# Kernel tuning notes

Measured on AMD Instinct MI355X. Metric: run time of the kernel, lower is better.

Reference implementation:

```python
import jax, jax.numpy as jnp
import numpy as np

DT = 0.01
NJ = 7
GRAV = 9.81
Q_LOWER = jnp.array([-2.9671, -1.8326, -2.9671, -3.1416, -2.9671, -0.0873, -2.9671], jnp.float32)
Q_UPPER = jnp.array([ 2.9671,  1.8326,  2.9671,  0.0,     2.9671,  3.8223,  2.9671], jnp.float32)


def _skew(v):
    z = jnp.zeros((), v.dtype)
    return jnp.stack([jnp.stack([z, -v[2], v[1]]),
                      jnp.stack([v[2], z, -v[0]]),
                      jnp.stack([-v[1], v[0], z])])


def _mot_X(E, r):
    # 6x6 spatial motion transform [[E,0],[-E*skew(r),E]]
    zero = jnp.zeros_like(E)
    top = jnp.concatenate([E, zero], axis=1)
    bot = jnp.concatenate([-E @ _skew(r), E], axis=1)
    return jnp.concatenate([top, bot], axis=0)


def _crm(v):
    # spatial motion cross-product matrix for v=[w;v0]
    Sw, Sv = _skew(v[:3]), _skew(v[3:])
    zero = jnp.zeros_like(Sw)
    top = jnp.concatenate([Sw, zero], axis=1)
    bot = jnp.concatenate([Sv, Sw], axis=1)
    return jnp.concatenate([top, bot], axis=0)


def _step_single(x, u, axes, R_tree, p_tree, I_sp):
    dt_ = x.dtype
    q = jnp.clip(x[:NJ], Q_LOWER.astype(dt_), Q_UPPER.astype(dt_))
    qd = x[NJ:]
    # forward kinematics: per-joint 6x6 child<-parent transforms and motion subspaces
    Xups, Ss = [], []
    eye3 = jnp.eye(3, dtype=dt_)
    for i in range(NJ):
        a = axes[i]
        c, s = jnp.cos(q[i]), jnp.sin(q[i])
        R = c * eye3 + s * _skew(a) + (1.0 - c) * jnp.outer(a, a)  # rodrigues
        Xj = _mot_X(R.T, jnp.zeros(3, dt_))
        Xt = _mot_X(R_tree[i], p_tree[i])
        Xups.append(Xj @ Xt)
        Ss.append(jnp.concatenate([a, jnp.zeros(3, dt_)]))
    # RNEA bias force h (qdd=0, gravity, zero base velocity, identity base pose)
    v_prev = jnp.zeros(6, dt_)
    a_prev = jnp.array([0.0, 0.0, 0.0, 0.0, 0.0, GRAV], dt_)  # a_base = -g trick
    fs = []
    for i in range(NJ):
        vJ = Ss[i] * qd[i]
        v = Xups[i] @ v_prev + vJ
        acc = Xups[i] @ a_prev + _crm(v) @ vJ
        Iv = I_sp[i] @ v
        f = I_sp[i] @ acc - _crm(v).T @ Iv  # crf(v) = -crm(v)^T
        fs.append(f)
        v_prev, a_prev = v, acc
    h = [None] * NJ
    for i in range(NJ - 1, -1, -1):
        h[i] = Ss[i] @ fs[i]
        if i > 0:
            fs[i - 1] = fs[i - 1] + Xups[i].T @ fs[i]
    h = jnp.stack(h)
    # CRBA mass matrix (serial chain, parent(i)=i-1)
    Ic = [I_sp[i] for i in range(NJ)]
    M = jnp.zeros((NJ, NJ), dt_)
    for i in range(NJ - 1, -1, -1):
        if i > 0:
            Ic[i - 1] = Ic[i - 1] + Xups[i].T @ Ic[i] @ Xups[i]
        F = Ic[i] @ Ss[i]
        M = M.at[i, i].set(Ss[i] @ F)
        for j in range(i - 1, -1, -1):
            F = Xups[j + 1].T @ F
            mij = Ss[j] @ F
            M = M.at[i, j].set(mij).at[j, i].set(mij)
    M = M + 1e-8 * jnp.eye(NJ, dtype=dt_)
    qdd = jnp.linalg.solve(M, (u - h)[:, None])[:, 0]
    qd_new = qd + DT * qdd
    q_new = q + DT * qd_new
    return jnp.concatenate([q_new, qd_new])


def setup_inputs() -> dict:
    B = 65536
    key = jax.random.key(0)
    k1, k2 = jax.random.split(key)
    x = jax.random.normal(k1, (B, 14), jnp.float32)
    u = jax.random.normal(k2, (B, 7), jnp.float32)
    rng = np.random.default_rng(0)
    # unit joint axes
    axes = rng.normal(size=(NJ, 3))
    axes = axes / np.linalg.norm(axes, axis=1, keepdims=True)
    # orthonormal fixed parent->child rotations (det +1)
    R_tree = np.empty((NJ, 3, 3))
    for i in range(NJ):
        Q, _ = np.linalg.qr(rng.normal(size=(3, 3)))
        if np.linalg.det(Q) < 0:
            Q[:, 0] = -Q[:, 0]
        R_tree[i] = Q
    p_tree = 0.2 * rng.normal(size=(NJ, 3))
    # SPD 6x6 spatial inertias: [[Ibar, m*Cx],[m*Cx^T, m*I3]]
    I_sp = np.empty((NJ, 6, 6))
    for i in range(NJ):
        m = float(rng.uniform(1.0, 5.0))
        c = 0.05 * rng.normal(size=3)
        Cx = np.array([[0, -c[2], c[1]], [c[2], 0, -c[0]], [-c[1], c[0], 0]])
        A = 0.1 * rng.normal(size=(3, 3))
        Ic_ = A @ A.T + 0.05 * np.eye(3)
        Ibar = Ic_ + m * Cx @ Cx.T
        I_sp[i] = np.block([[Ibar, m * Cx], [m * Cx.T, m * np.eye(3)]])
    return {
        "x": x, "u": u,
        "axes": jnp.asarray(axes, jnp.float32),
        "R_tree": jnp.asarray(R_tree, jnp.float32),
        "p_tree": jnp.asarray(p_tree, jnp.float32),
        "I_sp": jnp.asarray(I_sp, jnp.float32),
    }


def reference(x, u, axes, R_tree, p_tree, I_sp):
    return jax.vmap(_step_single, in_axes=(0, 0, None, None, None, None))(
        x, u, axes, R_tree, p_tree, I_sp)
```

## Files before the change

### kernel.cpp

```cpp
#include <hip/hip_runtime.h>
#include <math.h>

#define NJ 7
#define DTF 0.01f
#define GRAVF 9.81f
#define MIX(i,j) ((i)*((i)+1)/2 + (j))
#define MPAD 29
#define FSTR 43
#define SNC  15
#define QST  9

__device__ __forceinline__ void cross3(const float* a, const float* b, float* o){
    o[0] = a[1]*b[2] - a[2]*b[1];
    o[1] = a[2]*b[0] - a[0]*b[2];
    o[2] = a[0]*b[1] - a[1]*b[0];
}
__device__ __forceinline__ void mv3(const float* E, const float* x, float* y){
    y[0] = E[0]*x[0] + E[1]*x[1] + E[2]*x[2];
    y[1] = E[3]*x[0] + E[4]*x[1] + E[5]*x[2];
    y[2] = E[6]*x[0] + E[7]*x[1] + E[8]*x[2];
}
__device__ __forceinline__ void mtv3(const float* E, const float* x, float* y){
    y[0] = E[0]*x[0] + E[3]*x[1] + E[6]*x[2];
    y[1] = E[1]*x[0] + E[4]*x[1] + E[7]*x[2];
    y[2] = E[2]*x[0] + E[5]*x[1] + E[8]*x[2];
}
__device__ __forceinline__ void symv(const float* S, const float* x, float* y){
    y[0] = S[0]*x[0] + S[1]*x[1] + S[2]*x[2];
    y[1] = S[1]*x[0] + S[3]*x[1] + S[4]*x[2];
    y[2] = S[2]*x[0] + S[4]*x[1] + S[5]*x[2];
}
__device__ __forceinline__ void mm3(const float* A, const float* B, float* o){
#pragma unroll
    for (int r = 0; r < 3; r++)
#pragma unroll
        for (int c = 0; c < 3; c++)
            o[r*3+c] = A[r*3]*B[c] + A[r*3+1]*B[3+c] + A[r*3+2]*B[6+c];
}
__device__ __forceinline__ void congr(const float* E, const float* X, float* o){
    float t[9];
#pragma unroll
    for (int r = 0; r < 3; r++)
#pragma unroll
        for (int c = 0; c < 3; c++)
            t[r*3+c] = E[r]*X[c] + E[3+r]*X[3+c] + E[6+r]*X[6+c];
    mm3(t, E, o);
}
__device__ __forceinline__ void makeE(const float* a, const float* __restrict__ Rt,
                                      float s, float c, float* E){
    float omc = 1.0f - c;
    float RT[9];
    RT[0] = c + omc*a[0]*a[0];       RT[1] =  s*a[2] + omc*a[0]*a[1]; RT[2] = -s*a[1] + omc*a[0]*a[2];
    RT[3] = -s*a[2] + omc*a[1]*a[0]; RT[4] = c + omc*a[1]*a[1];       RT[5] =  s*a[0] + omc*a[1]*a[2];
    RT[6] =  s*a[1] + omc*a[2]*a[0]; RT[7] = -s*a[0] + omc*a[2]*a[1]; RT[8] = c + omc*a[2]*a[2];
    float Rl[9];
#pragma unroll
    for (int k = 0; k < 9; k++) Rl[k] = Rt[k];
    mm3(RT, Rl, E);
}
__device__ __forceinline__ void bodyI(const float* __restrict__ g_I, int i,
                                      float* SA, float* h, float& m){
    const float* I6 = g_I + i*36;
    SA[0]=I6[0]; SA[1]=I6[1]; SA[2]=I6[2];
    SA[3]=I6[7]; SA[4]=I6[8]; SA[5]=I6[14];
    h[0]=I6[16]; h[1]=I6[5]; h[2]=I6[9];
    m = I6[21];
}

__constant__ float QL_c[NJ] = {-2.9671f,-1.8326f,-2.9671f,-3.1416f,-2.9671f,-0.0873f,-2.9671f};
__constant__ float QU_c[NJ] = { 2.9671f, 1.8326f, 2.9671f, 0.0f,    2.9671f, 3.8223f, 2.9671f};

__global__ __launch_bounds__(128)
void panda_step(const float* __restrict__ x, const float* __restrict__ u,
                const float* __restrict__ g_ax, const float* __restrict__ g_Rt,
                const float* __restrict__ g_pt, const float* __restrict__ g_I,
                float* __restrict__ out, int B)
{
    __shared__ float s_M[64*MPAD];
    __shared__ float s_F[2*64*FSTR];
    __shared__ float s_snc[64*SNC];
    __shared__ float s_qd[64*QST];
    __shared__ float s_rhs[64*QST];

    const int role = threadIdx.x >> 6;
    const int lane = threadIdx.x & 63;
    const int e    = blockIdx.x*64 + lane;
    const bool act = (e < B);

    float q[NJ], qd[NJ];
    if (act && role == 0){
        float xl[14];
        const float2* x2 = (const float2*)(x + e*14);
#pragma unroll
        for (int i = 0; i < 7; i++){ float2 v = x2[i]; xl[2*i] = v.x; xl[2*i+1] = v.y; }
#pragma unroll
        for (int i = 0; i < NJ; i++){
            q[i]  = fminf(fmaxf(xl[i], QL_c[i]), QU_c[i]);
            qd[i] = xl[NJ + i];
            float s, c; __sincosf(q[i], &s, &c);
            s_snc[lane*SNC + i]     = s;
            s_snc[lane*SNC + 7 + i] = c;
            s_qd[lane*QST + i]      = qd[i];
            s_rhs[lane*QST + i]     = u[e*NJ + i];
        }
    }
    __syncthreads();

    if (act && role == 1){
        float* Fb = &s_F[64*FSTR + lane*FSTR];
        float SA[6], hc[3], mc;
        bodyI(g_I, 6, SA, hc, mc);
#pragma unroll 1
        for (int i = NJ-1; i >= 0; --i){
            float a[3] = { g_ax[3*i], g_ax[3*i+1], g_ax[3*i+2] };
            float p[3] = { g_pt[3*i], g_pt[3*i+1], g_pt[3*i+2] };
            float Ft[3]; symv(SA, a, Ft);
            Fb[i*6+0]=Ft[0]; Fb[i*6+1]=Ft[1]; Fb[i*6+2]=Ft[2];
            Fb[i*6+3] = a[1]*hc[2] - a[2]*hc[1];
            Fb[i*6+4] = a[2]*hc[0] - a[0]*hc[2];
            Fb[i*6+5] = a[0]*hc[1] - a[1]*hc[0];
#pragma unroll 1
            for (int k = i; k < NJ; ++k){
                float f0=Fb[k*6], f1=Fb[k*6+1], f2=Fb[k*6+2];
                s_M[lane*MPAD + k*(k+1)/2 + i] = a[0]*f0 + a[1]*f1 + a[2]*f2;
            }
            if (i > 0){
                float snv = s_snc[lane*SNC+i], csv = s_snc[lane*SNC+7+i];
                float E[9]; makeE(a, g_Rt + 9*i, snv, csv, E);
                float SAm[6], hm[3], mm_;
                bodyI(g_I, i-1, SAm, hm, mm_);
                float Af[9] = {SA[0],SA[1],SA[2], SA[1],SA[3],SA[4], SA[2],SA[4],SA[5]};
                float Ap[9]; congr(E, Af, Ap);
                float hr[3]; mtv3(E, hc, hr);
                float hpd = hr[0]*p[0]+hr[1]*p[1]+hr[2]*p[2];
                float ppd = p[0]*p[0]+p[1]*p[1]+p[2]*p[2];
                float dga = 2.0f*hpd + mc*ppd;
                SA[0] = Ap[0] - 2.0f*p[0]*hr[0] - mc*p[0]*p[0] + dga + SAm[0];
                SA[1] = Ap[1] - p[0]*hr[1] - hr[0]*p[1] - mc*p[0]*p[1] + SAm[1];
                SA[2] = Ap[2] - p[0]*hr[2] - hr[0]*p[2] - mc*p[0]*p[2] + SAm[2];
                SA[3] = Ap[4] - 2.0f*p[1]*hr[1] - mc*p[1]*p[1] + dga + SAm[3];
                SA[4] = Ap[5] - p[1]*hr[2] - hr[1]*p[2] - mc*p[1]*p[2] + SAm[4];
                SA[5] = Ap[8] - 2.0f*p[2]*hr[2] - mc*p[2]*p[2] + dga + SAm[5];
                hc[0] = hr[0] + mc*p[0] + hm[0];
                hc[1] = hr[1] + mc*p[1] + hm[1];
                hc[2] = hr[2] + mc*p[2] + hm[2];
                mc += mm_;
#pragma unroll 1
                for (int k = i; k < NJ; ++k){
                    float ft[3] = {Fb[k*6+0], Fb[k*6+1], Fb[k*6+2]};
                    float fb[3] = {Fb[k*6+3], Fb[k*6+4], Fb[k*6+5]};
                    float tm[3], tf[3], cp[3];
                    mtv3(E, ft, tm); mtv3(E, fb, tf);
                    cross3(p, tf, cp);
                    Fb[k*6+0]=tm[0]+cp[0]; Fb[k*6+1]=tm[1]+cp[1]; Fb[k*6+2]=tm[2]+cp[2];
                    Fb[k*6+3]=tf[0];       Fb[k*6+4]=tf[1];       Fb[k*6+5]=tf[2];
                }
            }
        }
        float Mx[28];
#pragma unroll
        for (int j = 0; j < 28; j++) Mx[j] = s_M[lane*MPAD + j];
#pragma unroll
        for (int i = 0; i < NJ; i++) Mx[MIX(i,i)] += 1e-8f;
#pragma unroll
        for (int k = 0; k < NJ; k++){
            float d = Mx[MIX(k,k)];
#pragma unroll
            for (int j = 0; j < NJ; j++) if (j < k) d -= Mx[MIX(k,j)]*Mx[MIX(k,j)];
            float linv = __builtin_amdgcn_rsqf(d);
            Mx[MIX(k,k)] = linv;
#pragma unroll
            for (int i2 = k+1; i2 < NJ; i2++){
                float s2 = Mx[MIX(i2,k)];
#pragma unroll
                for (int j = 0; j < NJ; j++) if (j < k) s2 -= Mx[MIX(i2,j)]*Mx[MIX(k,j)];
                Mx[MIX(i2,k)] = s2 * linv;
            }
        }
#pragma unroll
        for (int j = 0; j < 28; j++) s_M[lane*MPAD + j] = Mx[j];
    }
    else if (act){
        float* Fb = &s_F[lane*FSTR];
        float w[3]  = {0.f,0.f,0.f}, vl[3] = {0.f,0.f,0.f};
        float aw[3] = {0.f,0.f,0.f}, av[3] = {0.f,0.f,GRAVF};
#pragma unroll 1
        for (int i = 0; i < NJ; ++i){
            float a[3] = { g_ax[3*i], g_ax[3*i+1], g_ax[3*i+2] };
            float p[3] = { g_pt[3*i], g_pt[3*i+1], g_pt[3*i+2] };
            float snv = s_snc[lane*SNC+i], csv = s_snc[lane*SNC+7+i];
            float qdi = s_qd[lane*QST+i];
            float E[9]; makeE(a, g_Rt + 9*i, snv, csv, E);
            float tw[3]; mv3(E, w, tw);
            float nw[3] = { tw[0]+a[0]*qdi, tw[1]+a[1]*qdi, tw[2]+a[2]*qdi };
            float cwp[3]; cross3(w, p, cwp);
            float t1[3] = { vl[0]+cwp[0], vl[1]+cwp[1], vl[2]+cwp[2] };
            float nvl[3]; mv3(E, t1, nvl);
            float taw[3]; mv3(E, aw, taw);
            float cna[3]; cross3(nw, a, cna);
            float naw[3] = { taw[0]+qdi*cna[0], taw[1]+qdi*cna[1], taw[2]+qdi*cna[2] };
            float cap[3]; cross3(aw, p, cap);
            float t2[3] = { av[0]+cap[0], av[1]+cap[1], av[2]+cap[2] };
            float tav[3]; mv3(E, t2, tav);
            float cva[3]; cross3(nvl, a, cva);
            float nav[3] = { tav[0]+qdi*cva[0], tav[1]+qdi*cva[1], tav[2]+qdi*cva[2] };
            float SAi[6], hi[3], mi; bodyI(g_I, i, SAi, hi, mi);
            float Ivt[3], Iat[3], hxv[3], hxa[3];
            symv(SAi, nw, Ivt);  cross3(hi, nvl, hxv);
            symv(SAi, naw, Iat); cross3(hi, nav, hxa);
#pragma unroll
            for (int k = 0; k < 3; k++){ Ivt[k] += hxv[k]; Iat[k] += hxa[k]; }
            float hxw[3], hxaw[3];
            cross3(hi, nw, hxw); cross3(hi, naw, hxaw);
            float Ivb[3] = { mi*nvl[0]-hxw[0], mi*nvl[1]-hxw[1], mi*nvl[2]-hxw[2] };
            float Iab[3] = { mi*nav[0]-hxaw[0], mi*nav[1]-hxaw[1], mi*nav[2]-hxaw[2] };
            float c1[3], c2[3], c3[3];
            cross3(nw, Ivt, c1); cross3(nvl, Ivb, c2); cross3(nw, Ivb, c3);
            Fb[i*6+0] = Iat[0]+c1[0]+c2[0];
            Fb[i*6+1] = Iat[1]+c1[1]+c2[1];
            Fb[i*6+2] = Iat[2]+c1[2]+c2[2];
            Fb[i*6+3] = Iab[0]+c3[0];
            Fb[i*6+4] = Iab[1]+c3[1];
            Fb[i*6+5] = Iab[2]+c3[2];
#pragma unroll
            for (int k = 0; k < 3; k++){ w[k]=nw[k]; vl[k]=nvl[k]; aw[k]=naw[k]; av[k]=nav[k]; }
        }
#pragma unroll 1
        for (int i = NJ-1; i >= 0; --i){
            float a[3] = { g_ax[3*i], g_ax[3*i+1], g_ax[3*i+2] };
            float f0=Fb[i*6+0], f1=Fb[i*6+1], f2=Fb[i*6+2];
            s_rhs[lane*QST+i] -= a[0]*f0 + a[1]*f1 + a[2]*f2;
            if (i > 0){
                float p[3] = { g_pt[3*i], g_pt[3*i+1], g_pt[3*i+2] };
                float snv = s_snc[lane*SNC+i], csv = s_snc[lane*SNC+7+i];
                float E[9]; makeE(a, g_Rt + 9*i, snv, csv, E);
                float ftop[3] = {f0, f1, f2};
                float fbot[3] = {Fb[i*6+3], Fb[i*6+4], Fb[i*6+5]};
                float tm[3], tf[3], cp[3];
                mtv3(E, ftop, tm); mtv3(E, fbot, tf);
                cross3(p, tf, cp);
                Fb[(i-1)*6+0] += tm[0]+cp[0];
                Fb[(i-1)*6+1] += tm[1]+cp[1];
                Fb[(i-1)*6+2] += tm[2]+cp[2];
                Fb[(i-1)*6+3] += tf[0];
                Fb[(i-1)*6+4] += tf[1];
                Fb[(i-1)*6+5] += tf[2];
            }
        }
    }

    __syncthreads();

    if (act && role == 0){
        float Mx[28];
#pragma unroll
        for (int j = 0; j < 28; j++) Mx[j] = s_M[lane*MPAD + j];
        float rhs[NJ];
#pragma unroll
        for (int i = 0; i < NJ; i++) rhs[i] = s_rhs[lane*QST + i];
        float y[NJ];
#pragma unroll
        for (int i = 0; i < NJ; i++){
            float s2 = rhs[i];
#pragma unroll
            for (int j = 0; j < NJ; j++) if (j < i) s2 -= Mx[MIX(i,j)]*y[j];
            y[i] = s2 * Mx[MIX(i,i)];
        }
        float z[NJ];
#pragma unroll
        for (int i = NJ-1; i >= 0; i--){
            float s2 = y[i];
#pragma unroll
            for (int j = NJ-1; j >= 0; j--) if (j > i) s2 -= Mx[MIX(j,i)]*z[j];
            z[i] = s2 * Mx[MIX(i,i)];
        }
        float o14[14];
#pragma unroll
        for (int i = 0; i < NJ; i++){
            float qdn = qd[i] + DTF*z[i];
            o14[i]      = q[i] + DTF*qdn;
            o14[NJ + i] = qdn;
        }
        float2* o2 = (float2*)(out + e*14);
#pragma unroll
        for (int i = 0; i < 7; i++){ float2 v; v.x = o14[2*i]; v.y = o14[2*i+1]; o2[i] = v; }
    }
}

extern "C" void kernel_launch(void* const* d_in, const int* in_sizes, int n_in,
                              void* d_out, int out_size, void* d_ws, size_t ws_size,
                              hipStream_t stream) {
    const float* x   = (const float*)d_in[0];
    const float* u   = (const float*)d_in[1];
    const float* ax  = (const float*)d_in[2];
    const float* Rt  = (const float*)d_in[3];
    const float* pt  = (const float*)d_in[4];
    const float* Isp = (const float*)d_in[5];
    float* out = (float*)d_out;
    int B = in_sizes[0] / 14;
    int grid = (B + 63) / 64;
    hipLaunchKernelGGL(panda_step, dim3(grid), dim3(128), 0, stream,
                       x, u, ax, Rt, pt, Isp, out, B);
}
```

Measured before the change: 78.58 us.

## Replace RNEA+CRBA+Cholesky with Featherstone articulated-body algorithm per thread

```diff
diff --git a/kernel.cpp b/kernel.cpp
--- a/kernel.cpp
+++ b/kernel.cpp
@@ -4,11 +4,16 @@
 #define NJ 7
 #define DTF 0.01f
 #define GRAVF 9.81f
-#define MIX(i,j) ((i)*((i)+1)/2 + (j))
-#define MPAD 29
-#define FSTR 43
-#define SNC  15
-#define QST  9
+
+#define S_SN(i)    (i)
+#define S_CS(i)    (7 + (i))
+#define S_QD(i)    (14 + (i))
+#define S_TAU(i)   (21 + (i))
+#define S_VU(i,k)  (28 + 6*(i) + (k))
+#define S_CC(i,k)  (70 + 6*(i) + (k))
+#define S_DI(i)    (112 + (i))
+#define S_UU(i)    (119 + (i))
+#define NSLOT 126
 
 __device__ __forceinline__ void cross3(const float* a, const float* b, float* o){
     o[0] = a[1]*b[2] - a[2]*b[1];
@@ -37,14 +42,38 @@
         for (int c = 0; c < 3; c++)
             o[r*3+c] = A[r*3]*B[c] + A[r*3+1]*B[3+c] + A[r*3+2]*B[6+c];
 }
+__device__ __forceinline__ void mtm3(const float* A, const float* B, float* o){
+#pragma unroll
+    for (int r = 0; r < 3; r++)
+#pragma unroll
+        for (int c = 0; c < 3; c++)
+            o[r*3+c] = A[r]*B[c] + A[3+r]*B[3+c] + A[6+r]*B[6+c];
+}
 __device__ __forceinline__ void congr(const float* E, const float* X, float* o){
     float t[9];
-#pragma unroll
-    for (int r = 0; r < 3; r++)
-#pragma unroll
-        for (int c = 0; c < 3; c++)
-            t[r*3+c] = E[r]*X[c] + E[3+r]*X[3+c] + E[6+r]*X[6+c];
+    mtm3(E, X, t);
     mm3(t, E, o);
+}
+__device__ __forceinline__ void skewR(const float* M, const float* p, float* O){
+#pragma unroll
+    for (int r = 0; r < 3; r++){
+        O[r*3+0] = M[r*3+1]*p[2] - M[r*3+2]*p[1];
+        O[r*3+1] = M[r*3+2]*p[0] - M[r*3+0]*p[2];
+        O[r*3+2] = M[r*3+0]*p[1] - M[r*3+1]*p[0];
+    }
+}
+__device__ __forceinline__ void skewL(const float* p, const float* M, float* O){
+#pragma unroll
+    for (int c = 0; c < 3; c++){
+        O[0*3+c] = p[1]*M[2*3+c] - p[2]*M[1*3+c];
+        O[1*3+c] = p[2]*M[0*3+c] - p[0]*M[2*3+c];
+        O[2*3+c] = p[0]*M[1*3+c] - p[1]*M[0*3+c];
+    }
+}
+__device__ __forceinline__ void symexp(const float* S, float* F){
+    F[0]=S[0]; F[1]=S[1]; F[2]=S[2];
+    F[3]=S[1]; F[4]=S[3]; F[5]=S[4];
+    F[6]=S[2]; F[7]=S[4]; F[8]=S[5];
 }
 __device__ __forceinline__ void makeE(const float* a, const float* __restrict__ Rt,
                                       float s, float c, float* E){
@@ -70,25 +99,20 @@
 __constant__ float QL_c[NJ] = {-2.9671f,-1.8326f,-2.9671f,-3.1416f,-2.9671f,-0.0873f,-2.9671f};
 __constant__ float QU_c[NJ] = { 2.9671f, 1.8326f, 2.9671f, 0.0f,    2.9671f, 3.8223f, 2.9671f};
 
-__global__ __launch_bounds__(128)
+__global__ __launch_bounds__(64, 1)
 void panda_step(const float* __restrict__ x, const float* __restrict__ u,
                 const float* __restrict__ g_ax, const float* __restrict__ g_Rt,
                 const float* __restrict__ g_pt, const float* __restrict__ g_I,
                 float* __restrict__ out, int B)
 {
-    __shared__ float s_M[64*MPAD];
-    __shared__ float s_F[2*64*FSTR];
-    __shared__ float s_snc[64*SNC];
-    __shared__ float s_qd[64*QST];
-    __shared__ float s_rhs[64*QST];
-
-    const int role = threadIdx.x >> 6;
-    const int lane = threadIdx.x & 63;
+    __shared__ float s_buf[NSLOT*64];
+    const int lane = threadIdx.x;
     const int e    = blockIdx.x*64 + lane;
-    const bool act = (e < B);
+    if (e >= B) return;
+#define SL(idx) s_buf[(idx)*64 + lane]
 
     float q[NJ], qd[NJ];
-    if (act && role == 0){
+    {
         float xl[14];
         const float2* x2 = (const float2*)(x + e*14);
 #pragma unroll
@@ -98,186 +122,167 @@
             q[i]  = fminf(fmaxf(xl[i], QL_c[i]), QU_c[i]);
             qd[i] = xl[NJ + i];
             float s, c; __sincosf(q[i], &s, &c);
-            s_snc[lane*SNC + i]     = s;
-            s_snc[lane*SNC + 7 + i] = c;
-            s_qd[lane*QST + i]      = qd[i];
-            s_rhs[lane*QST + i]     = u[e*NJ + i];
-        }
-    }
-    __syncthreads();
-
-    if (act && role == 1){
-        float* Fb = &s_F[64*FSTR + lane*FSTR];
-        float SA[6], hc[3], mc;
-        bodyI(g_I, 6, SA, hc, mc);
-#pragma unroll 1
-        for (int i = NJ-1; i >= 0; --i){
-            float a[3] = { g_ax[3*i], g_ax[3*i+1], g_ax[3*i+2] };
-            float p[3] = { g_pt[3*i], g_pt[3*i+1], g_pt[3*i+2] };
-            float Ft[3]; symv(SA, a, Ft);
-            Fb[i*6+0]=Ft[0]; Fb[i*6+1]=Ft[1]; Fb[i*6+2]=Ft[2];
-            Fb[i*6+3] = a[1]*hc[2] - a[2]*hc[1];
-            Fb[i*6+4] = a[2]*hc[0] - a[0]*hc[2];
-            Fb[i*6+5] = a[0]*hc[1] - a[1]*hc[0];
-#pragma unroll 1
-            for (int k = i; k < NJ; ++k){
-                float f0=Fb[k*6], f1=Fb[k*6+1], f2=Fb[k*6+2];
-                s_M[lane*MPAD + k*(k+1)/2 + i] = a[0]*f0 + a[1]*f1 + a[2]*f2;
-            }
-            if (i > 0){
-                float snv = s_snc[lane*SNC+i], csv = s_snc[lane*SNC+7+i];
-                float E[9]; makeE(a, g_Rt + 9*i, snv, csv, E);
-                float SAm[6], hm[3], mm_;
-                bodyI(g_I, i-1, SAm, hm, mm_);
-                float Af[9] = {SA[0],SA[1],SA[2], SA[1],SA[3],SA[4], SA[2],SA[4],SA[5]};
-                float Ap[9]; congr(E, Af, Ap);
-                float hr[3]; mtv3(E, hc, hr);
-                float hpd = hr[0]*p[0]+hr[1]*p[1]+hr[2]*p[2];
-                float ppd = p[0]*p[0]+p[1]*p[1]+p[2]*p[2];
-                float dga = 2.0f*hpd + mc*ppd;
-                SA[0] = Ap[0] - 2.0f*p[0]*hr[0] - mc*p[0]*p[0] + dga + SAm[0];
-                SA[1] = Ap[1] - p[0]*hr[1] - hr[0]*p[1] - mc*p[0]*p[1] + SAm[1];
-                SA[2] = Ap[2] - p[0]*hr[2] - hr[0]*p[2] - mc*p[0]*p[2] + SAm[2];
-                SA[3] = Ap[4] - 2.0f*p[1]*hr[1] - mc*p[1]*p[1] + dga + SAm[3];
-                SA[4] = Ap[5] - p[1]*hr[2] - hr[1]*p[2] - mc*p[1]*p[2] + SAm[4];
-                SA[5] = Ap[8] - 2.0f*p[2]*hr[2] - mc*p[2]*p[2] + dga + SAm[5];
-                hc[0] = hr[0] + mc*p[0] + hm[0];
-                hc[1] = hr[1] + mc*p[1] + hm[1];
-                hc[2] = hr[2] + mc*p[2] + hm[2];
-                mc += mm_;
-#pragma unroll 1
-                for (int k = i; k < NJ; ++k){
-                    float ft[3] = {Fb[k*6+0], Fb[k*6+1], Fb[k*6+2]};
-                    float fb[3] = {Fb[k*6+3], Fb[k*6+4], Fb[k*6+5]};
-                    float tm[3], tf[3], cp[3];
-                    mtv3(E, ft, tm); mtv3(E, fb, tf);
-                    cross3(p, tf, cp);
-                    Fb[k*6+0]=tm[0]+cp[0]; Fb[k*6+1]=tm[1]+cp[1]; Fb[k*6+2]=tm[2]+cp[2];
-                    Fb[k*6+3]=tf[0];       Fb[k*6+4]=tf[1];       Fb[k*6+5]=tf[2];
-                }
-            }
-        }
-        float Mx[28];
-#pragma unroll
-        for (int j = 0; j < 28; j++) Mx[j] = s_M[lane*MPAD + j];
-#pragma unroll
-        for (int i = 0; i < NJ; i++) Mx[MIX(i,i)] += 1e-8f;
-#pragma unroll
-        for (int k = 0; k < NJ; k++){
-            float d = Mx[MIX(k,k)];
-#pragma unroll
-            for (int j = 0; j < NJ; j++) if (j < k) d -= Mx[MIX(k,j)]*Mx[MIX(k,j)];
-            float linv = __builtin_amdgcn_rsqf(d);
-            Mx[MIX(k,k)] = linv;
-#pragma unroll
-            for (int i2 = k+1; i2 < NJ; i2++){
-                float s2 = Mx[MIX(i2,k)];
-#pragma unroll
-                for (int j = 0; j < NJ; j++) if (j < k) s2 -= Mx[MIX(i2,j)]*Mx[MIX(k,j)];
-                Mx[MIX(i2,k)] = s2 * linv;
-            }
-        }
-#pragma unroll
-        for (int j = 0; j < 28; j++) s_M[lane*MPAD + j] = Mx[j];
-    }
-    else if (act){
-        float* Fb = &s_F[lane*FSTR];
-        float w[3]  = {0.f,0.f,0.f}, vl[3] = {0.f,0.f,0.f};
-        float aw[3] = {0.f,0.f,0.f}, av[3] = {0.f,0.f,GRAVF};
+            SL(S_SN(i))  = s;
+            SL(S_CS(i))  = c;
+            SL(S_QD(i))  = qd[i];
+            SL(S_TAU(i)) = u[e*NJ + i];
+        }
+    }
+
+    {
+        float w[3] = {0.f,0.f,0.f}, vl[3] = {0.f,0.f,0.f};
 #pragma unroll 1
         for (int i = 0; i < NJ; ++i){
             float a[3] = { g_ax[3*i], g_ax[3*i+1], g_ax[3*i+2] };
             float p[3] = { g_pt[3*i], g_pt[3*i+1], g_pt[3*i+2] };
-            float snv = s_snc[lane*SNC+i], csv = s_snc[lane*SNC+7+i];
-            float qdi = s_qd[lane*QST+i];
-            float E[9]; makeE(a, g_Rt + 9*i, snv, csv, E);
-            float tw[3]; mv3(E, w, tw);
-            float nw[3] = { tw[0]+a[0]*qdi, tw[1]+a[1]*qdi, tw[2]+a[2]*qdi };
+            float sn = SL(S_SN(i)), cs = SL(S_CS(i)), qdi = SL(S_QD(i));
+            float E[9]; makeE(a, g_Rt + 9*i, sn, cs, E);
             float cwp[3]; cross3(w, p, cwp);
-            float t1[3] = { vl[0]+cwp[0], vl[1]+cwp[1], vl[2]+cwp[2] };
-            float nvl[3]; mv3(E, t1, nvl);
-            float taw[3]; mv3(E, aw, taw);
-            float cna[3]; cross3(nw, a, cna);
-            float naw[3] = { taw[0]+qdi*cna[0], taw[1]+qdi*cna[1], taw[2]+qdi*cna[2] };
-            float cap[3]; cross3(aw, p, cap);
-            float t2[3] = { av[0]+cap[0], av[1]+cap[1], av[2]+cap[2] };
-            float tav[3]; mv3(E, t2, tav);
-            float cva[3]; cross3(nvl, a, cva);
-            float nav[3] = { tav[0]+qdi*cva[0], tav[1]+qdi*cva[1], tav[2]+qdi*cva[2] };
-            float SAi[6], hi[3], mi; bodyI(g_I, i, SAi, hi, mi);
-            float Ivt[3], Iat[3], hxv[3], hxa[3];
-            symv(SAi, nw, Ivt);  cross3(hi, nvl, hxv);
-            symv(SAi, naw, Iat); cross3(hi, nav, hxa);
-#pragma unroll
-            for (int k = 0; k < 3; k++){ Ivt[k] += hxv[k]; Iat[k] += hxa[k]; }
-            float hxw[3], hxaw[3];
-            cross3(hi, nw, hxw); cross3(hi, naw, hxaw);
-            float Ivb[3] = { mi*nvl[0]-hxw[0], mi*nvl[1]-hxw[1], mi*nvl[2]-hxw[2] };
-            float Iab[3] = { mi*nav[0]-hxaw[0], mi*nav[1]-hxaw[1], mi*nav[2]-hxaw[2] };
-            float c1[3], c2[3], c3[3];
-            cross3(nw, Ivt, c1); cross3(nvl, Ivb, c2); cross3(nw, Ivb, c3);
-            Fb[i*6+0] = Iat[0]+c1[0]+c2[0];
-            Fb[i*6+1] = Iat[1]+c1[1]+c2[1];
-            Fb[i*6+2] = Iat[2]+c1[2]+c2[2];
-            Fb[i*6+3] = Iab[0]+c3[0];
-            Fb[i*6+4] = Iab[1]+c3[1];
-            Fb[i*6+5] = Iab[2]+c3[2];
-#pragma unroll
-            for (int k = 0; k < 3; k++){ w[k]=nw[k]; vl[k]=nvl[k]; aw[k]=naw[k]; av[k]=nav[k]; }
+            float t[3] = { vl[0]+cwp[0], vl[1]+cwp[1], vl[2]+cwp[2] };
+            float nw[3], nl[3];
+            mv3(E, w, nw); mv3(E, t, nl);
+            nw[0] += a[0]*qdi; nw[1] += a[1]*qdi; nw[2] += a[2]*qdi;
+#pragma unroll
+            for (int k = 0; k < 3; k++){
+                SL(S_VU(i,k))   = nw[k];
+                SL(S_VU(i,3+k)) = nl[k];
+                w[k] = nw[k]; vl[k] = nl[k];
+            }
+        }
+    }
+
+    {
+        float A[6], Bm[9], C[6];
+        float px[6] = {0.f,0.f,0.f,0.f,0.f,0.f};
+        {
+            float SA[6], h[3], m; bodyI(g_I, NJ-1, SA, h, m);
+#pragma unroll
+            for (int k = 0; k < 6; k++) A[k] = SA[k];
+            Bm[0]=0.f;    Bm[1]=-h[2]; Bm[2]= h[1];
+            Bm[3]= h[2];  Bm[4]=0.f;   Bm[5]=-h[0];
+            Bm[6]=-h[1];  Bm[7]= h[0]; Bm[8]=0.f;
+            C[0]=m; C[1]=0.f; C[2]=0.f; C[3]=m; C[4]=0.f; C[5]=m;
         }
 #pragma unroll 1
         for (int i = NJ-1; i >= 0; --i){
             float a[3] = { g_ax[3*i], g_ax[3*i+1], g_ax[3*i+2] };
-            float f0=Fb[i*6+0], f1=Fb[i*6+1], f2=Fb[i*6+2];
-            s_rhs[lane*QST+i] -= a[0]*f0 + a[1]*f1 + a[2]*f2;
+            float w[3], vl[3];
+#pragma unroll
+            for (int k = 0; k < 3; k++){ w[k] = SL(S_VU(i,k)); vl[k] = SL(S_VU(i,3+k)); }
+            float qdi = SL(S_QD(i)), taui = SL(S_TAU(i));
+            float SAi[6], hi[3], mi; bodyI(g_I, i, SAi, hi, mi);
+            float Ivt[3], hxl[3]; symv(SAi, w, Ivt); cross3(hi, vl, hxl);
+#pragma unroll
+            for (int k = 0; k < 3; k++) Ivt[k] += hxl[k];
+            float hxw[3]; cross3(hi, w, hxw);
+            float Ivb[3] = { mi*vl[0]-hxw[0], mi*vl[1]-hxw[1], mi*vl[2]-hxw[2] };
+            float c1[3], c2[3], c3[3];
+            cross3(w, Ivt, c1); cross3(vl, Ivb, c2); cross3(w, Ivb, c3);
+            float pAt[3] = { c1[0]+c2[0]+px[0], c1[1]+c2[1]+px[1], c1[2]+c2[2]+px[2] };
+            float pAb[3] = { c3[0]+px[3], c3[1]+px[4], c3[2]+px[5] };
+            float Ut[3], Ub[3];
+            symv(A, a, Ut); mtv3(Bm, a, Ub);
+            float d = a[0]*Ut[0] + a[1]*Ut[1] + a[2]*Ut[2];
+            float dinv = __builtin_amdgcn_rcpf(d);
+            float uu = taui - (a[0]*pAt[0] + a[1]*pAt[1] + a[2]*pAt[2]);
+#pragma unroll
+            for (int k = 0; k < 3; k++){ SL(S_VU(i,k)) = Ut[k]; SL(S_VU(i,3+k)) = Ub[k]; }
+            SL(S_DI(i)) = dinv;
+            SL(S_UU(i)) = uu;
+            float wxa[3], lxa[3]; cross3(w, a, wxa); cross3(vl, a, lxa);
+            float ct[3] = { qdi*wxa[0], qdi*wxa[1], qdi*wxa[2] };
+            float cb[3] = { qdi*lxa[0], qdi*lxa[1], qdi*lxa[2] };
+#pragma unroll
+            for (int k = 0; k < 3; k++){ SL(S_CC(i,k)) = ct[k]; SL(S_CC(i,3+k)) = cb[k]; }
             if (i > 0){
                 float p[3] = { g_pt[3*i], g_pt[3*i+1], g_pt[3*i+2] };
-                float snv = s_snc[lane*SNC+i], csv = s_snc[lane*SNC+7+i];
-                float E[9]; makeE(a, g_Rt + 9*i, snv, csv, E);
-                float ftop[3] = {f0, f1, f2};
-                float fbot[3] = {Fb[i*6+3], Fb[i*6+4], Fb[i*6+5]};
+                float sn = SL(S_SN(i)), cs = SL(S_CS(i));
+                float E[9]; makeE(a, g_Rt + 9*i, sn, cs, E);
+                float rA[6], rB[9], rC[6];
+                rA[0]=A[0]-dinv*Ut[0]*Ut[0]; rA[1]=A[1]-dinv*Ut[0]*Ut[1]; rA[2]=A[2]-dinv*Ut[0]*Ut[2];
+                rA[3]=A[3]-dinv*Ut[1]*Ut[1]; rA[4]=A[4]-dinv*Ut[1]*Ut[2]; rA[5]=A[5]-dinv*Ut[2]*Ut[2];
+#pragma unroll
+                for (int r = 0; r < 3; r++)
+#pragma unroll
+                    for (int c = 0; c < 3; c++)
+                        rB[r*3+c] = Bm[r*3+c] - dinv*Ut[r]*Ub[c];
+                rC[0]=C[0]-dinv*Ub[0]*Ub[0]; rC[1]=C[1]-dinv*Ub[0]*Ub[1]; rC[2]=C[2]-dinv*Ub[0]*Ub[2];
+                rC[3]=C[3]-dinv*Ub[1]*Ub[1]; rC[4]=C[4]-dinv*Ub[1]*Ub[2]; rC[5]=C[5]-dinv*Ub[2]*Ub[2];
+                float du = dinv*uu;
+                float t1[3], t2[3];
+                symv(rA, ct, t1); mv3(rB, cb, t2);
+                float pat[3] = { pAt[0]+t1[0]+t2[0]+du*Ut[0],
+                                 pAt[1]+t1[1]+t2[1]+du*Ut[1],
+                                 pAt[2]+t1[2]+t2[2]+du*Ut[2] };
+                mtv3(rB, ct, t1); symv(rC, cb, t2);
+                float pab[3] = { pAb[0]+t1[0]+t2[0]+du*Ub[0],
+                                 pAb[1]+t1[1]+t2[1]+du*Ub[1],
+                                 pAb[2]+t1[2]+t2[2]+du*Ub[2] };
+                float Ff[9], AeF[9], CeF[9], tB[9], Bf[9];
+                symexp(rA, Ff); congr(E, Ff, AeF);
+                symexp(rC, Ff); congr(E, Ff, CeF);
+                mtm3(E, rB, tB); mm3(tB, E, Bf);
+                float Bp[9], Qm[9], PQ[9], LC[9];
+                skewR(Bf, p, Bp);
+                skewR(CeF, p, Qm); skewL(p, Qm, PQ);
+                skewL(p, CeF, LC);
+                float SAm[6], hm[3], mm_; bodyI(g_I, i-1, SAm, hm, mm_);
+                A[0] = SAm[0] + AeF[0] - 2.0f*Bp[0]     - PQ[0];
+                A[1] = SAm[1] + AeF[1] - (Bp[1]+Bp[3])  - PQ[1];
+                A[2] = SAm[2] + AeF[2] - (Bp[2]+Bp[6])  - PQ[2];
+                A[3] = SAm[3] + AeF[4] - 2.0f*Bp[4]     - PQ[4];
+                A[4] = SAm[4] + AeF[5] - (Bp[5]+Bp[7])  - PQ[5];
+                A[5] = SAm[5] + AeF[8] - 2.0f*Bp[8]     - PQ[8];
+                Bm[0] = Bf[0]+LC[0];        Bm[1] = Bf[1]+LC[1]-hm[2]; Bm[2] = Bf[2]+LC[2]+hm[1];
+                Bm[3] = Bf[3]+LC[3]+hm[2];  Bm[4] = Bf[4]+LC[4];       Bm[5] = Bf[5]+LC[5]-hm[0];
+                Bm[6] = Bf[6]+LC[6]-hm[1];  Bm[7] = Bf[7]+LC[7]+hm[0]; Bm[8] = Bf[8]+LC[8];
+                C[0] = mm_ + CeF[0]; C[1] = CeF[1]; C[2] = CeF[2];
+                C[3] = mm_ + CeF[4]; C[4] = CeF[5]; C[5] = mm_ + CeF[8];
                 float tm[3], tf[3], cp[3];
-                mtv3(E, ftop, tm); mtv3(E, fbot, tf);
+                mtv3(E, pat, tm); mtv3(E, pab, tf);
                 cross3(p, tf, cp);
-                Fb[(i-1)*6+0] += tm[0]+cp[0];
-                Fb[(i-1)*6+1] += tm[1]+cp[1];
-                Fb[(i-1)*6+2] += tm[2]+cp[2];
-                Fb[(i-1)*6+3] += tf[0];
-                Fb[(i-1)*6+4] += tf[1];
-                Fb[(i-1)*6+5] += tf[2];
+                px[0]=tm[0]+cp[0]; px[1]=tm[1]+cp[1]; px[2]=tm[2]+cp[2];
+                px[3]=tf[0];       px[4]=tf[1];       px[5]=tf[2];
             }
         }
     }
 
-    __syncthreads();
-
-    if (act && role == 0){
-        float Mx[28];
-#pragma unroll
-        for (int j = 0; j < 28; j++) Mx[j] = s_M[lane*MPAD + j];
-        float rhs[NJ];
-#pragma unroll
-        for (int i = 0; i < NJ; i++) rhs[i] = s_rhs[lane*QST + i];
-        float y[NJ];
+    {
+        float at[3] = {0.f,0.f,0.f}, ab[3] = {0.f,0.f,GRAVF};
+#pragma unroll 1
+        for (int i = 0; i < NJ; ++i){
+            float a[3] = { g_ax[3*i], g_ax[3*i+1], g_ax[3*i+2] };
+            float p[3] = { g_pt[3*i], g_pt[3*i+1], g_pt[3*i+2] };
+            float sn = SL(S_SN(i)), cs = SL(S_CS(i));
+            float E[9]; makeE(a, g_Rt + 9*i, sn, cs, E);
+            float axp[3]; cross3(at, p, axp);
+            float t[3] = { ab[0]+axp[0], ab[1]+axp[1], ab[2]+axp[2] };
+            float apt[3], apb[3];
+            mv3(E, at, apt); mv3(E, t, apb);
+#pragma unroll
+            for (int k = 0; k < 3; k++){
+                apt[k] += SL(S_CC(i,k));
+                apb[k] += SL(S_CC(i,3+k));
+            }
+            float Ut[3] = { SL(S_VU(i,0)), SL(S_VU(i,1)), SL(S_VU(i,2)) };
+            float Ub[3] = { SL(S_VU(i,3)), SL(S_VU(i,4)), SL(S_VU(i,5)) };
+            float dinv = SL(S_DI(i)), uu = SL(S_UU(i));
+            float qdd = dinv*(uu - (Ut[0]*apt[0]+Ut[1]*apt[1]+Ut[2]*apt[2]
+                                   + Ub[0]*apb[0]+Ub[1]*apb[1]+Ub[2]*apb[2]));
+            SL(S_TAU(i)) = qdd;
+            at[0] = apt[0] + a[0]*qdd;
+            at[1] = apt[1] + a[1]*qdd;
+            at[2] = apt[2] + a[2]*qdd;
+            ab[0] = apb[0]; ab[1] = apb[1]; ab[2] = apb[2];
+        }
+    }
+
+    {
+        float o14[14];
 #pragma unroll
         for (int i = 0; i < NJ; i++){
-            float s2 = rhs[i];
-#pragma unroll
-            for (int j = 0; j < NJ; j++) if (j < i) s2 -= Mx[MIX(i,j)]*y[j];
-            y[i] = s2 * Mx[MIX(i,i)];
-        }
-        float z[NJ];
-#pragma unroll
-        for (int i = NJ-1; i >= 0; i--){
-            float s2 = y[i];
-#pragma unroll
-            for (int j = NJ-1; j >= 0; j--) if (j > i) s2 -= Mx[MIX(j,i)]*z[j];
-            z[i] = s2 * Mx[MIX(i,i)];
-        }
-        float o14[14];
-#pragma unroll
-        for (int i = 0; i < NJ; i++){
-            float qdn = qd[i] + DTF*z[i];
+            float qdd = SL(S_TAU(i));
+            float qdn = qd[i] + DTF*qdd;
             o14[i]      = q[i] + DTF*qdn;
             o14[NJ + i] = qdn;
         }
@@ -285,6 +290,7 @@
 #pragma unroll
         for (int i = 0; i < 7; i++){ float2 v; v.x = o14[2*i]; v.y = o14[2*i+1]; o2[i] = v; }
     }
+#undef SL
 }
 
 extern "C" void kernel_launch(void* const* d_in, const int* in_sizes, int n_in,
@@ -299,6 +305,6 @@
     float* out = (float*)d_out;
     int B = in_sizes[0] / 14;
     int grid = (B + 63) / 64;
-    hipLaunchKernelGGL(panda_step, dim3(grid), dim3(128), 0, stream,
+    hipLaunchKernelGGL(panda_step, dim3(grid), dim3(64), 0, stream,
                        x, u, ax, Rt, pt, Isp, out, B);
 }
```

Result: slower. 81.19 us (+3.3%).
